# Optimization experiments

Measured on AMD Instinct MI355X. Metric: run time of the kernel, lower is better.

The kernel has to match this reference:

```python
import jax, jax.numpy as jnp
import numpy as np

N = 8192
IN_F = 512
NFEAT = 512
OUT_F = 512


def setup_inputs() -> dict:
    key = jax.random.key(0)
    k1, k2, k3, k4, k5 = jax.random.split(key, 5)
    stdv = 1.0 / np.sqrt(OUT_F)
    return {
        "input": jax.random.normal(k1, (N, IN_F), dtype=jnp.float32),
        "adj": jax.random.uniform(k2, (N, N), dtype=jnp.float32),
        "x": jax.random.normal(k3, (N, NFEAT), dtype=jnp.float32),
        "weight": jax.random.uniform(k4, (IN_F + N + NFEAT, OUT_F), minval=-stdv, maxval=stdv, dtype=jnp.float32),
        "bias": jax.random.uniform(k5, (OUT_F,), minval=-stdv, maxval=stdv, dtype=jnp.float32),
    }


def reference(input, adj, x, weight, bias):
    # support = [adj @ input | adj | x]  -> [n, in_features + n + nfeat]
    support = jnp.concatenate((adj @ input, adj, x), axis=1)
    return support @ weight + bias
```

## Files before the change

kernel.cpp:

```cpp
#include <hip/hip_runtime.h>
#include <hip/hip_bf16.h>

typedef __attribute__((ext_vector_type(4))) float f32x4;
typedef __attribute__((ext_vector_type(8))) short bf16x8;
typedef __attribute__((ext_vector_type(4))) unsigned short u16x4;
typedef __attribute__((ext_vector_type(8))) unsigned short u16x8;

__device__ __forceinline__ unsigned short f2bf(float f) {
    unsigned int u = __builtin_bit_cast(unsigned int, f);
    u += 0x7fffu + ((u >> 16) & 1u);
    return (unsigned short)(u >> 16);
}

#define SWZ(i) ((i) ^ ((((i) >> 6) & 7) << 3))

constexpr int BM = 64, BN = 128, BK = 64;

__global__ void transpose_cvt(const float* __restrict__ src,
                              unsigned short* __restrict__ dst,
                              int rows, int cols) {
    int idx = blockIdx.x * 256 + threadIdx.x;
    int n = idx / rows;
    int k = idx - n * rows;
    unsigned short v = f2bf(src[(size_t)k * cols + n]);
    int ntile = n >> 7, ktile = k >> 6;
    dst[((size_t)(ntile * (rows >> 6) + ktile)) * 8192 +
        SWZ((n & 127) * 64 + (k & 63))] = v;
}

template<int EPI>
__global__ __launch_bounds__(512, 4)
void gemm_k(const float* __restrict__ A, long lda,
            const unsigned short* __restrict__ Bt,
            int K,
            const float* __restrict__ epi, long lde,
            const float* __restrict__ bias,
            void* __restrict__ Dptr, long ldd) {
    __shared__ unsigned short sA[2][BM * BK];
    __shared__ unsigned short sB[2][BN * BK];

    const int t = threadIdx.x;
    const int l = t & 63;
    const int w = t >> 6;
    const int wm = w >> 2;
    const int wn = w & 3;

    int mt, nt;
    {
        int lin = blockIdx.y * gridDim.x + blockIdx.x;
        int xcd = lin & 7;
        int slot = lin >> 3;
        int ppx = gridDim.y >> 3;
        mt = xcd * ppx + slot / gridDim.x;
        nt = slot % gridDim.x;
    }
    const long m0 = (long)mt * BM;
    const long n0 = (long)nt * BN;
    const int KT = K >> 6;
    const unsigned short* Bblk = Bt + (size_t)nt * KT * 8192;

    f32x4 acc[2][2];
    #pragma unroll
    for (int m = 0; m < 2; ++m)
        #pragma unroll
        for (int n = 0; n < 2; ++n)
            acc[m][n] = {0.f, 0.f, 0.f, 0.f};

    f32x4 aX0, aX1, aY0, aY1;

    auto gll_B = [&](int kt, int buf) {
        const unsigned short* src = Bblk + (size_t)kt * 8192 + t * 8;
        #pragma unroll
        for (int r = 0; r < 2; ++r) {
            __builtin_amdgcn_global_load_lds(
                (const __attribute__((address_space(1))) void*)(src + r * 4096),
                (__attribute__((address_space(3))) void*)&sB[buf][r * 4096 + w * 512],
                16, 0, 0);
        }
    };

    auto load_A = [&](int kt, f32x4& a0, f32x4& a1) {
        const float* p0 = &A[(m0 + (t >> 4)) * lda + (long)kt * BK + ((t & 15) << 2)];
        const float* p1 = p0 + 32 * lda;
        asm volatile("global_load_dwordx4 %0, %2, off\n\t"
                     "global_load_dwordx4 %1, %3, off"
                     : "=&v"(a0), "=&v"(a1)
                     : "v"(p0), "v"(p1)
                     : "memory");
    };

    auto write_A = [&](int buf, const f32x4& a0, const f32x4& a1) {
        int e0 = t * 4;
        u16x4 w0 = {f2bf(a0[0]), f2bf(a0[1]), f2bf(a0[2]), f2bf(a0[3])};
        *reinterpret_cast<u16x4*>(&sA[buf][SWZ(e0)]) = w0;
        int e1 = 2048 + t * 4;
        u16x4 w1 = {f2bf(a1[0]), f2bf(a1[1]), f2bf(a1[2]), f2bf(a1[3])};
        *reinterpret_cast<u16x4*>(&sA[buf][SWZ(e1)]) = w1;
    };

    auto compute = [&](int buf) {
        #pragma unroll
        for (int kk = 0; kk < 2; ++kk) {
            bf16x8 af[2], bfr[2];
            const int kb = kk * 32 + ((l >> 4) << 3);
            #pragma unroll
            for (int m = 0; m < 2; ++m) {
                int row = wm * 32 + m * 16 + (l & 15);
                af[m] = *reinterpret_cast<const bf16x8*>(&sA[buf][SWZ(row * 64 + kb)]);
            }
            #pragma unroll
            for (int n = 0; n < 2; ++n) {
                int col = wn * 32 + n * 16 + (l & 15);
                bfr[n] = *reinterpret_cast<const bf16x8*>(&sB[buf][SWZ(col * 64 + kb)]);
            }
            __builtin_amdgcn_s_setprio(1);
            #pragma unroll
            for (int m = 0; m < 2; ++m)
                #pragma unroll
                for (int n = 0; n < 2; ++n)
                    acc[m][n] = __builtin_amdgcn_mfma_f32_16x16x32_bf16(
                        af[m], bfr[n], acc[m][n], 0, 0, 0);
            __builtin_amdgcn_s_setprio(0);
        }
    };

    gll_B(0, 0);
    load_A(0, aX0, aX1);
    load_A(1, aY0, aY1);
    asm volatile("s_waitcnt vmcnt(2)" ::: "memory");
    __builtin_amdgcn_sched_barrier(0);
    write_A(0, aX0, aX1);
    asm volatile("s_waitcnt lgkmcnt(0)" ::: "memory");
    __builtin_amdgcn_s_barrier();
    __builtin_amdgcn_sched_barrier(0);

    const int nk = K >> 6;
    for (int p = 0; p + 2 < nk; p += 2) {
        gll_B(p + 1, 1);
        load_A(p + 2, aX0, aX1);
        compute(0);
        asm volatile("s_waitcnt vmcnt(4)" ::: "memory");
        __builtin_amdgcn_sched_barrier(0);
        write_A(1, aY0, aY1);
        asm volatile("s_waitcnt vmcnt(2) lgkmcnt(0)" ::: "memory");
        __builtin_amdgcn_s_barrier();
        __builtin_amdgcn_sched_barrier(0);

        gll_B(p + 2, 0);
        load_A(p + 3, aY0, aY1);
        compute(1);
        asm volatile("s_waitcnt vmcnt(4)" ::: "memory");
        __builtin_amdgcn_sched_barrier(0);
        write_A(0, aX0, aX1);
        asm volatile("s_waitcnt vmcnt(2) lgkmcnt(0)" ::: "memory");
        __builtin_amdgcn_s_barrier();
        __builtin_amdgcn_sched_barrier(0);
    }

    gll_B(nk - 1, 1);
    compute(0);
    asm volatile("s_waitcnt vmcnt(2)" ::: "memory");
    __builtin_amdgcn_sched_barrier(0);
    write_A(1, aY0, aY1);
    asm volatile("s_waitcnt vmcnt(0) lgkmcnt(0)" ::: "memory");
    __builtin_amdgcn_s_barrier();
    __builtin_amdgcn_sched_barrier(0);

    compute(1);

    const int jrow = (l >> 4) * 4;
    #pragma unroll
    for (int m = 0; m < 2; ++m) {
        const long row = m0 + wm * 32 + m * 16 + jrow;
        #pragma unroll
        for (int n = 0; n < 2; ++n) {
            const long col = n0 + wn * 32 + n * 16 + (l & 15);
            f32x4 v = acc[m][n];
            if constexpr (EPI == 0) {
                u16x4 o;
                #pragma unroll
                for (int j = 0; j < 4; ++j)
                    o[j] = f2bf(v[j] + epi[(row + j) * lde + col]);
                int ntile = (int)(col >> 7), cl = (int)(col & 127);
                int ktile = (int)(row >> 6), kk = (int)(row & 63);
                *reinterpret_cast<u16x4*>(
                    &((unsigned short*)Dptr)[((size_t)(ntile * (int)ldd + ktile)) * 8192 +
                                             SWZ(cl * 64 + kk)]) = o;
            } else if constexpr (EPI == 1) {
                float b = bias[col];
                #pragma unroll
                for (int j = 0; j < 4; ++j)
                    ((float*)Dptr)[(row + j) * ldd + col] = v[j] + b;
            } else {
                #pragma unroll
                for (int j = 0; j < 4; ++j)
                    ((float*)Dptr)[(row + j) * ldd + col] =
                        v[j] + epi[(row + j) * lde + col];
            }
        }
    }
}

extern "C" void kernel_launch(void* const* d_in, const int* in_sizes, int n_in,
                              void* d_out, int out_size, void* d_ws, size_t ws_size,
                              hipStream_t stream) {
    const float* input  = (const float*)d_in[0];
    const float* adj    = (const float*)d_in[1];
    const float* x      = (const float*)d_in[2];
    const float* weight = (const float*)d_in[3];
    const float* bias   = (const float*)d_in[4];

    const int N = 8192, IN_F = 512, NFEAT = 512, OUT_F = 512;
    float* out = (float*)d_out;

    unsigned short* Tbt = (unsigned short*)d_ws;
    unsigned short* W1t = Tbt + (size_t)OUT_F * N;
    unsigned short* W3t = W1t + (size_t)OUT_F * IN_F;
    float* C0 = (float*)(W3t + (size_t)OUT_F * NFEAT);

    transpose_cvt<<<dim3((IN_F * OUT_F) / 256), dim3(256), 0, stream>>>(
        weight, W1t, IN_F, OUT_F);
    transpose_cvt<<<dim3((NFEAT * OUT_F) / 256), dim3(256), 0, stream>>>(
        weight + (size_t)(IN_F + N) * OUT_F, W3t, NFEAT, OUT_F);

    dim3 grid(OUT_F / BN, N / BM);

    gemm_k<0><<<grid, 512, 0, stream>>>(
        input, (long)IN_F, W1t, IN_F,
        weight + (size_t)IN_F * OUT_F, (long)OUT_F, nullptr,
        Tbt, (long)(N / 64));

    gemm_k<1><<<grid, 512, 0, stream>>>(
        x, (long)NFEAT, W3t, NFEAT,
        nullptr, 0, bias,
        C0, (long)OUT_F);

    gemm_k<2><<<grid, 512, 0, stream>>>(
        adj, (long)N, Tbt, N,
        C0, (long)OUT_F, nullptr,
        out, (long)OUT_F);
}
```

Before: 186.4 us.

## Replace big adj GEMM with 256x256 split-K kernel accumulating via atomics

Adds a dedicated gemm_big kernel for the dominant adj @ T product. It uses 256x256 output tiles, 4x8 MFMA fragments per wave, and a 4-way split-K, with partial results added into the output through float atomic adds. The x@W3+bias GEMM now writes directly into the output first, so the intermediate C0 buffer and the epilogue-add kernel are gone, and Tbt is re-laid out in 256-wide tiles. This raises data reuse and cuts A re-reads of the 8192x8192 adj matrix. In exchange it adds atomic traffic, a nondeterministic summation order, and a grid of only 256 blocks with heavy register use.

New measurement: 248.7 us. 33.4% more time.

```diff
diff --git a/kernel.cpp b/kernel.cpp
--- a/kernel.cpp
+++ b/kernel.cpp
@@ -14,30 +14,28 @@
 
 #define SWZ(i) ((i) ^ ((((i) >> 6) & 7) << 3))
 
-constexpr int BM = 64, BN = 128, BK = 64;
-
 __global__ void transpose_cvt(const float* __restrict__ src,
                               unsigned short* __restrict__ dst,
-                              int rows, int cols) {
+                              int rows, int cols, int ltw) {
     int idx = blockIdx.x * 256 + threadIdx.x;
     int n = idx / rows;
     int k = idx - n * rows;
     unsigned short v = f2bf(src[(size_t)k * cols + n]);
-    int ntile = n >> 7, ktile = k >> 6;
-    dst[((size_t)(ntile * (rows >> 6) + ktile)) * 8192 +
-        SWZ((n & 127) * 64 + (k & 63))] = v;
+    int tw = 1 << ltw;
+    int tile = (n >> ltw) * (rows >> 6) + (k >> 6);
+    dst[(size_t)tile * (tw * 64) + SWZ((n & (tw - 1)) * 64 + (k & 63))] = v;
 }
 
 template<int EPI>
 __global__ __launch_bounds__(512, 4)
-void gemm_k(const float* __restrict__ A, long lda,
-            const unsigned short* __restrict__ Bt,
-            int K,
-            const float* __restrict__ epi, long lde,
-            const float* __restrict__ bias,
-            void* __restrict__ Dptr, long ldd) {
-    __shared__ unsigned short sA[2][BM * BK];
-    __shared__ unsigned short sB[2][BN * BK];
+void gemm_small(const float* __restrict__ A, long lda,
+                const unsigned short* __restrict__ Bt,
+                int K,
+                const float* __restrict__ epi, long lde,
+                const float* __restrict__ bias,
+                void* __restrict__ Dptr, long ldd) {
+    __shared__ unsigned short sA[2][64 * 64];
+    __shared__ unsigned short sB[2][128 * 64];
 
     const int t = threadIdx.x;
     const int l = t & 63;
@@ -54,8 +52,8 @@
         mt = xcd * ppx + slot / gridDim.x;
         nt = slot % gridDim.x;
     }
-    const long m0 = (long)mt * BM;
-    const long n0 = (long)nt * BN;
+    const long m0 = (long)mt * 64;
+    const long n0 = (long)nt * 128;
     const int KT = K >> 6;
     const unsigned short* Bblk = Bt + (size_t)nt * KT * 8192;
 
@@ -71,16 +69,15 @@
     auto gll_B = [&](int kt, int buf) {
         const unsigned short* src = Bblk + (size_t)kt * 8192 + t * 8;
         #pragma unroll
-        for (int r = 0; r < 2; ++r) {
+        for (int r = 0; r < 2; ++r)
             __builtin_amdgcn_global_load_lds(
                 (const __attribute__((address_space(1))) void*)(src + r * 4096),
                 (__attribute__((address_space(3))) void*)&sB[buf][r * 4096 + w * 512],
                 16, 0, 0);
-        }
     };
 
     auto load_A = [&](int kt, f32x4& a0, f32x4& a1) {
-        const float* p0 = &A[(m0 + (t >> 4)) * lda + (long)kt * BK + ((t & 15) << 2)];
+        const float* p0 = &A[(m0 + (t >> 4)) * lda + (long)kt * 64 + ((t & 15) << 2)];
         const float* p1 = p0 + 32 * lda;
         asm volatile("global_load_dwordx4 %0, %2, off\n\t"
                      "global_load_dwordx4 %1, %3, off"
@@ -165,7 +162,6 @@
     asm volatile("s_waitcnt vmcnt(0) lgkmcnt(0)" ::: "memory");
     __builtin_amdgcn_s_barrier();
     __builtin_amdgcn_sched_barrier(0);
-
     compute(1);
 
     const int jrow = (l >> 4) * 4;
@@ -181,22 +177,157 @@
                 #pragma unroll
                 for (int j = 0; j < 4; ++j)
                     o[j] = f2bf(v[j] + epi[(row + j) * lde + col]);
-                int ntile = (int)(col >> 7), cl = (int)(col & 127);
-                int ktile = (int)(row >> 6), kk = (int)(row & 63);
+                int tile = ((int)col >> 8) * 128 + ((int)row >> 6);
+                int idx = ((int)col & 255) * 64 + ((int)row & 63);
                 *reinterpret_cast<u16x4*>(
-                    &((unsigned short*)Dptr)[((size_t)(ntile * (int)ldd + ktile)) * 8192 +
-                                             SWZ(cl * 64 + kk)]) = o;
-            } else if constexpr (EPI == 1) {
+                    &((unsigned short*)Dptr)[(size_t)tile * 16384 + SWZ(idx)]) = o;
+            } else {
                 float b = bias[col];
                 #pragma unroll
                 for (int j = 0; j < 4; ++j)
                     ((float*)Dptr)[(row + j) * ldd + col] = v[j] + b;
-            } else {
+            }
+        }
+    }
+}
+
+__global__ __launch_bounds__(512, 2)
+void gemm_big(const float* __restrict__ A,
+              const unsigned short* __restrict__ Bt,
+              float* __restrict__ Out) {
+    __shared__ unsigned short sA[2][256 * 64];
+    __shared__ unsigned short sB[2][256 * 64];
+
+    const int t = threadIdx.x;
+    const int l = t & 63;
+    const int w = t >> 6;
+    const int wm = w & 3;
+    const int wn = w >> 2;
+
+    const int lin = blockIdx.x;
+    const int combo = lin & 7;
+    const int nt = combo & 1;
+    const int kq = combo >> 1;
+    const int mt = lin >> 3;
+
+    const long m0 = (long)mt * 256;
+    const long k0 = (long)kq * 2048;
+    const int n0 = nt * 256;
+    const int ktbase = nt * 128 + kq * 32;
+    constexpr int P = 32;
+
+    f32x4 acc[4][8];
+    #pragma unroll
+    for (int mi = 0; mi < 4; ++mi)
+        #pragma unroll
+        for (int ni = 0; ni < 8; ++ni)
+            acc[mi][ni] = {0.f, 0.f, 0.f, 0.f};
+
+    f32x4 avX[8], avY[8];
+
+    auto gll_B = [&](int ph, int buf) {
+        const unsigned short* src = Bt + ((size_t)(ktbase + ph)) * 16384 + t * 8;
+        #pragma unroll
+        for (int r = 0; r < 4; ++r)
+            __builtin_amdgcn_global_load_lds(
+                (const __attribute__((address_space(1))) void*)(src + r * 4096),
+                (__attribute__((address_space(3))) void*)&sB[buf][r * 4096 + w * 512],
+                16, 0, 0);
+    };
+
+    auto load_A = [&](int ph, f32x4* av) {
+        const float* base = A + m0 * 8192 + k0 + (long)ph * 64;
+        #pragma unroll
+        for (int j = 0; j < 8; ++j) {
+            int chunk = j * 512 + t;
+            int row = chunk >> 4;
+            int kc = (chunk & 15) << 2;
+            const float* p = base + (long)row * 8192 + kc;
+            asm volatile("global_load_dwordx4 %0, %1, off"
+                         : "=&v"(av[j]) : "v"(p) : "memory");
+        }
+    };
+
+    auto write_A = [&](int buf, const f32x4* av) {
+        #pragma unroll
+        for (int j = 0; j < 8; ++j) {
+            int chunk = j * 512 + t;
+            int row = chunk >> 4;
+            int kc = (chunk & 15) << 2;
+            int idx = row * 64 + kc;
+            u16x4 wv = {f2bf(av[j][0]), f2bf(av[j][1]), f2bf(av[j][2]), f2bf(av[j][3])};
+            *reinterpret_cast<u16x4*>(&sA[buf][SWZ(idx)]) = wv;
+        }
+    };
+
+    auto compute = [&](int buf) {
+        #pragma unroll
+        for (int kk = 0; kk < 2; ++kk) {
+            const int kb = kk * 32 + ((l >> 4) << 3);
+            bf16x8 af[4], bf[8];
+            #pragma unroll
+            for (int mi = 0; mi < 4; ++mi) {
+                int row = wm * 64 + mi * 16 + (l & 15);
+                af[mi] = *reinterpret_cast<const bf16x8*>(&sA[buf][SWZ(row * 64 + kb)]);
+            }
+            #pragma unroll
+            for (int ni = 0; ni < 8; ++ni) {
+                int col = wn * 128 + ni * 16 + (l & 15);
+                bf[ni] = *reinterpret_cast<const bf16x8*>(&sB[buf][SWZ(col * 64 + kb)]);
+            }
+            __builtin_amdgcn_s_setprio(1);
+            #pragma unroll
+            for (int mi = 0; mi < 4; ++mi)
                 #pragma unroll
-                for (int j = 0; j < 4; ++j)
-                    ((float*)Dptr)[(row + j) * ldd + col] =
-                        v[j] + epi[(row + j) * lde + col];
-            }
+                for (int ni = 0; ni < 8; ++ni)
+                    acc[mi][ni] = __builtin_amdgcn_mfma_f32_16x16x32_bf16(
+                        af[mi], bf[ni], acc[mi][ni], 0, 0, 0);
+            __builtin_amdgcn_s_setprio(0);
+        }
+    };
+
+    gll_B(0, 0);
+    load_A(0, avX);
+    asm volatile("s_waitcnt vmcnt(0)" ::: "memory");
+    __builtin_amdgcn_sched_barrier(0);
+    write_A(0, avX);
+    load_A(1, avX);
+    asm volatile("s_waitcnt lgkmcnt(0)" ::: "memory");
+    __builtin_amdgcn_s_barrier();
+    __builtin_amdgcn_sched_barrier(0);
+
+    for (int p = 0; p < P; p += 2) {
+        gll_B(p + 1 < P ? p + 1 : P - 1, (p + 1) & 1);
+        load_A(p + 2 < P ? p + 2 : P - 1, avY);
+        asm volatile("s_waitcnt vmcnt(12)" ::: "memory");
+        __builtin_amdgcn_sched_barrier(0);
+        write_A((p + 1) & 1, avX);
+        compute(p & 1);
+        asm volatile("s_waitcnt vmcnt(8) lgkmcnt(0)" ::: "memory");
+        __builtin_amdgcn_s_barrier();
+        __builtin_amdgcn_sched_barrier(0);
+
+        int q = p + 1;
+        gll_B(q + 1 < P ? q + 1 : P - 1, (q + 1) & 1);
+        load_A(q + 2 < P ? q + 2 : P - 1, avX);
+        asm volatile("s_waitcnt vmcnt(12)" ::: "memory");
+        __builtin_amdgcn_sched_barrier(0);
+        write_A((q + 1) & 1, avY);
+        compute(q & 1);
+        asm volatile("s_waitcnt vmcnt(8) lgkmcnt(0)" ::: "memory");
+        __builtin_amdgcn_s_barrier();
+        __builtin_amdgcn_sched_barrier(0);
+    }
+
+    #pragma unroll
+    for (int mi = 0; mi < 4; ++mi) {
+        const long row0 = m0 + wm * 64 + mi * 16 + ((l >> 4) << 2);
+        #pragma unroll
+        for (int ni = 0; ni < 8; ++ni) {
+            const int col = n0 + wn * 128 + ni * 16 + (l & 15);
+            #pragma unroll
+            for (int j = 0; j < 4; ++j)
+                unsafeAtomicAdd(&Out[(row0 + j) * 512 + col], acc[mi][ni][j]);
         }
     }
 }
@@ -214,29 +345,25 @@
     float* out = (float*)d_out;
 
     unsigned short* Tbt = (unsigned short*)d_ws;
-    unsigned short* W1t = Tbt + (size_t)OUT_F * N;
-    unsigned short* W3t = W1t + (size_t)OUT_F * IN_F;
-    float* C0 = (float*)(W3t + (size_t)OUT_F * NFEAT);
+    unsigned short* W1t = Tbt + (size_t)2 * 128 * 16384;
+    unsigned short* W3t = W1t + (size_t)4 * 8 * 8192;
 
     transpose_cvt<<<dim3((IN_F * OUT_F) / 256), dim3(256), 0, stream>>>(
-        weight, W1t, IN_F, OUT_F);
+        weight, W1t, IN_F, OUT_F, 7);
     transpose_cvt<<<dim3((NFEAT * OUT_F) / 256), dim3(256), 0, stream>>>(
-        weight + (size_t)(IN_F + N) * OUT_F, W3t, NFEAT, OUT_F);
-
-    dim3 grid(OUT_F / BN, N / BM);
-
-    gemm_k<0><<<grid, 512, 0, stream>>>(
+        weight + (size_t)(IN_F + N) * OUT_F, W3t, NFEAT, OUT_F, 7);
+
+    dim3 grid(OUT_F / 128, N / 64);
+
+    gemm_small<1><<<grid, 512, 0, stream>>>(
+        x, (long)NFEAT, W3t, NFEAT,
+        nullptr, 0, bias,
+        out, (long)OUT_F);
+
+    gemm_small<0><<<grid, 512, 0, stream>>>(
         input, (long)IN_F, W1t, IN_F,
         weight + (size_t)IN_F * OUT_F, (long)OUT_F, nullptr,
-        Tbt, (long)(N / 64));
-
-    gemm_k<1><<<grid, 512, 0, stream>>>(
-        x, (long)NFEAT, W3t, NFEAT,
-        nullptr, 0, bias,
-        C0, (long)OUT_F);
-
-    gemm_k<2><<<grid, 512, 0, stream>>>(
-        adj, (long)N, Tbt, N,
-        C0, (long)OUT_F, nullptr,
-        out, (long)OUT_F);
-}
+        Tbt, 0);
+
+    gemm_big<<<dim3(256), dim3(512), 0, stream>>>(adj, Tbt, out);
+}
```
